# Performance work log

Measured on AMD Instinct MI355X. Metric: run time of the kernel, lower is better.

The kernel has to match this reference:

```python
import jax, jax.numpy as jnp
import numpy as np


def setup_inputs() -> dict:
    key = jax.random.key(0)
    ks = jax.random.split(key, 7)
    N, D, C, SY, SX = 512, 256, 128, 12, 12
    return {
        "f_t": jax.random.normal(ks[0], (N, D), dtype=jnp.float32),
        "fmap_t": jax.random.normal(ks[1], (N, SY, SX, C), dtype=jnp.float32),
        "fmap_tp1": jax.random.normal(ks[2], (N, SY, SX, C), dtype=jnp.float32),
        "W1": jax.random.normal(ks[3], (C, D), dtype=jnp.float32) * 0.05,
        "b1": jax.random.normal(ks[4], (C,), dtype=jnp.float32) * 0.05,
        "W2": jax.random.normal(ks[5], (C, C), dtype=jnp.float32) * 0.05,
        "b2": jax.random.normal(ks[6], (C,), dtype=jnp.float32) * 0.05,
    }


def _ce_diag(logits):
    # logits: [L, N, N]; labels are arange(N) per location.
    lse = jax.nn.logsumexp(logits, axis=-1)           # [L, N]
    diag = jnp.diagonal(logits, axis1=1, axis2=2)     # [L, N]
    # mean over batch per location, then mean over locations == sum/L in torch code
    return jnp.mean(lse - diag)


def reference(f_t, fmap_t, fmap_tp1, W1, b1, W2, b2):
    N = f_t.shape[0]
    C = fmap_tp1.shape[-1]
    # flatten spatial grid: [L, N, C]
    pos = fmap_tp1.reshape(N, -1, C).transpose(1, 0, 2)
    loc = fmap_t.reshape(N, -1, C).transpose(1, 0, 2)

    # loss1: global-local. classifier1(f_t) is loop-invariant -> computed once.
    preds1 = f_t @ W1.T + b1                          # [N, C]
    logits1 = jnp.einsum('nc,lmc->lnm', preds1, pos)  # [L, N, N]
    loss1 = _ce_diag(logits1)

    # loss2: local-local, per-location linear fused as batched einsum.
    preds2 = jnp.einsum('lnc,dc->lnd', loc, W2) + b2  # [L, N, C]
    logits2 = jnp.einsum('lnc,lmc->lnm', preds2, pos) # [L, N, N]
    loss2 = _ce_diag(logits2)

    return loss1 + loss2
```

## Files before the change

### kernel.cpp

```cpp
#include <hip/hip_runtime.h>
#include <hip/hip_bf16.h>
#include <math.h>

#define LC 18432
#define LOG2E 1.4426950408889634f

typedef short bf16x8 __attribute__((ext_vector_type(8)));
typedef float f32x4 __attribute__((ext_vector_type(4)));

#define MFMA16 __builtin_amdgcn_mfma_f32_16x16x32_bf16

__device__ __forceinline__ float fast_exp2(float x) {
#if __has_builtin(__builtin_amdgcn_exp2f)
  return __builtin_amdgcn_exp2f(x);
#else
  return exp2f(x);
#endif
}
__device__ __forceinline__ float fast_log2(float x) {
#if __has_builtin(__builtin_amdgcn_logf)
  return __builtin_amdgcn_logf(x);
#else
  return log2f(x);
#endif
}

__device__ __forceinline__ ushort f2bf(float x) {
  __hip_bfloat16 h = __float2bfloat16(x);
  return __builtin_bit_cast(ushort, h);
}

__device__ __forceinline__ int swb(int row, int x) {
  return (row << 8) + (x ^ ((row & 15) << 4));
}
__device__ __forceinline__ int swb9(int row, int x) {
  return (row << 9) + (x ^ ((row & 15) << 4));
}

__global__ __launch_bounds__(256) void preds1_k(
    const float* __restrict__ f_t, const float* __restrict__ W1,
    const float* __restrict__ b1, ushort* __restrict__ p1img,
    float* __restrict__ out) {
  if (blockIdx.x == 0 && threadIdx.x == 0) *out = 0.f;
  __shared__ __align__(16) ushort sF[32 * 256];
  __shared__ __align__(16) ushort sW[64 * 256];
  const int rc = blockIdx.x >> 1, dh = blockIdx.x & 1;
  const int t = threadIdx.x;
  const int wave = t >> 6, lane = t & 63, lo = lane & 15, hi = lane >> 4;
#pragma unroll
  for (int k = 0; k < 8; ++k) {
    int idx = t + k * 256;
    int row = idx >> 6, c4 = (idx & 63) << 2;
    float4 v = *(const float4*)(f_t + (size_t)(rc * 32 + row) * 256 + c4);
    ushort4 h = {f2bf(v.x), f2bf(v.y), f2bf(v.z), f2bf(v.w)};
    *(ushort4*)((char*)sF + swb9(row, c4 << 1)) = h;
  }
#pragma unroll
  for (int k = 0; k < 16; ++k) {
    int idx = t + k * 256;
    int row = idx >> 6, c4 = (idx & 63) << 2;
    float4 v = *(const float4*)(W1 + (size_t)(dh * 64 + row) * 256 + c4);
    ushort4 h = {f2bf(v.x), f2bf(v.y), f2bf(v.z), f2bf(v.w)};
    *(ushort4*)((char*)sW + swb9(row, c4 << 1)) = h;
  }
  __syncthreads();
  const int rn = (wave & 1) * 16, wd = (wave >> 1) * 32;
  f32x4 acc[2] = {};
#pragma unroll
  for (int s = 0; s < 8; ++s) {
    int x = s * 64 + hi * 16;
    bf16x8 a = *(const bf16x8*)((const char*)sF + swb9(rn + lo, x));
#pragma unroll
    for (int j = 0; j < 2; ++j) {
      bf16x8 b = *(const bf16x8*)((const char*)sW + swb9(wd + j * 16 + lo, x));
      acc[j] = MFMA16(a, b, acc[j], 0, 0, 0);
    }
  }
#pragma unroll
  for (int j = 0; j < 2; ++j) {
    int d = dh * 64 + wd + j * 16 + lo;
    float bb = b1[d];
#pragma unroll
    for (int e = 0; e < 4; ++e) {
      int R = rc * 32 + rn + hi * 4 + e;
      int tile = R >> 6, rin = R & 63;
      *(ushort*)((char*)p1img + (size_t)tile * 16384 + (rin << 8) +
                 ((2 * d) ^ ((rin & 15) << 4))) =
          f2bf((acc[j][e] + bb) * LOG2E);
    }
  }
}

__device__ __forceinline__ void load_tile(float4 pv[4], const float* __restrict__ base,
                                          int t) {
#pragma unroll
  for (int k = 0; k < 4; ++k) {
    int idx = t + k * 512;
    int row = idx >> 5, c4 = (idx & 31) << 2;
    pv[k] = *(const float4*)(base + (size_t)row * LC + c4);
  }
}
__device__ __forceinline__ void write_tile(ushort* dstbuf, const float4 pv[4], int t) {
#pragma unroll
  for (int k = 0; k < 4; ++k) {
    int idx = t + k * 512;
    int row = idx >> 5, c4 = (idx & 31) << 2;
    ushort4 h = {f2bf(pv[k].x), f2bf(pv[k].y), f2bf(pv[k].z), f2bf(pv[k].w)};
    *(ushort4*)((char*)dstbuf + swb(row, c4 << 1)) = h;
  }
}

__global__ __launch_bounds__(512) void stdim_fused(
    const ushort* __restrict__ p1img, const float* __restrict__ fmap_t,
    const float* __restrict__ fmap_tp1, const float* __restrict__ W2,
    const float* __restrict__ b2, float* __restrict__ out) {
  __shared__ __align__(16) ushort sP[8192];
  __shared__ __align__(16) ushort sPos[16384];
  __shared__ float s_rows[2][64][2];
  __shared__ float s_diag[2][64];
  __shared__ float s_red[8];

  const int bid = blockIdx.x;
  const int work = (bid & 7) * 144 + (bid >> 3);
  const int l = work >> 3, rb = work & 7;
  const int t = threadIdx.x;
  const int wave = t >> 6, lane = t & 63, lo = lane & 15, hi = lane >> 4;
  const int ty_ = wave >> 2, wr = (wave >> 1) & 1, wc = wave & 1;

  const float* posbase = fmap_tp1 + l * 128;

#pragma unroll
  for (int k = 0; k < 4; ++k) {
    int idx = t + k * 512;
    int row = idx >> 5, c4 = (idx & 31) << 2;
    float4 v = *(const float4*)(fmap_t + (size_t)(rb * 64 + row) * LC + l * 128 + c4);
    ushort4 h = {f2bf(v.x), f2bf(v.y), f2bf(v.z), f2bf(v.w)};
    *(ushort4*)((char*)sP + swb(row, c4 << 1)) = h;
  }
#pragma unroll
  for (int k = 0; k < 8; ++k) {
    int idx = t + k * 512;
    int row = idx >> 5, c4 = (idx & 31) << 2;
    float4 v = *(const float4*)(W2 + (size_t)row * 128 + c4);
    ushort4 h = {f2bf(v.x), f2bf(v.y), f2bf(v.z), f2bf(v.w)};
    *(ushort4*)((char*)sPos + swb(row, c4 << 1)) = h;
  }
  const int wn = (wave & 1) * 32, wd = (wave >> 1) * 32;
  const float b2a = b2[wd + lo], b2b = b2[wd + 16 + lo];
  float4 pvA[4], pvB[4];
  load_tile(pvA, posbase, t);
  load_tile(pvB, posbase + (size_t)64 * LC, t);
  __syncthreads();

  f32x4 acc2[2][2] = {};
#pragma unroll
  for (int s = 0; s < 4; ++s) {
    int x = s * 64 + hi * 16;
    bf16x8 a0 = *(const bf16x8*)((const char*)sP + swb(wn + lo, x));
    bf16x8 a1 = *(const bf16x8*)((const char*)sP + swb(wn + 16 + lo, x));
#pragma unroll
    for (int j = 0; j < 2; ++j) {
      bf16x8 b = *(const bf16x8*)((const char*)sPos + swb(wd + j * 16 + lo, x));
      acc2[0][j] = MFMA16(a0, b, acc2[0][j], 0, 0, 0);
      acc2[1][j] = MFMA16(a1, b, acc2[1][j], 0, 0, 0);
    }
  }
  __syncthreads();

#pragma unroll
  for (int i2 = 0; i2 < 2; ++i2)
#pragma unroll
    for (int j = 0; j < 2; ++j)
#pragma unroll
      for (int e = 0; e < 4; ++e) {
        int r = wn + i2 * 16 + hi * 4 + e;
        int d = wd + j * 16 + lo;
        *(ushort*)((char*)sP + (r << 8) + ((2 * d) ^ ((r & 15) << 4))) =
            f2bf((acc2[i2][j][e] + (j ? b2b : b2a)) * LOG2E);
      }
  write_tile((ushort*)sPos, pvA, t);
  write_tile((ushort*)((char*)sPos + 16384), pvB, t);
  __syncthreads();

  bf16x8 af[2][4];
  if (ty_ == 0) {
    const char* aimg = (const char*)(p1img + (size_t)rb * 8192);
#pragma unroll
    for (int rt = 0; rt < 2; ++rt)
#pragma unroll
      for (int s = 0; s < 4; ++s)
        af[rt][s] = *(const bf16x8*)(aimg + swb(wr * 32 + rt * 16 + lo, s * 64 + hi * 16));
  } else {
#pragma unroll
    for (int rt = 0; rt < 2; ++rt)
#pragma unroll
      for (int s = 0; s < 4; ++s)
        af[rt][s] = *(const bf16x8*)((const char*)sP +
                                     swb(wr * 32 + rt * 16 + lo, s * 64 + hi * 16));
  }

  float sm0[4] = {0.f, 0.f, 0.f, 0.f}, sm1[4] = {0.f, 0.f, 0.f, 0.f};

#pragma unroll
  for (int mt = 0; mt < 8; ++mt) {
    float4 nv[4];
    if (mt < 6) load_tile(nv, posbase + (size_t)((mt + 2) * 64) * LC, t);

    const char* cur = (const char*)sPos + (mt & 1) * 16384;
    f32x4 a00 = {}, a01 = {}, a10 = {}, a11 = {};
#pragma unroll
    for (int s = 0; s < 4; ++s) {
      int x = s * 64 + hi * 16;
      bf16x8 b0 = *(const bf16x8*)(cur + swb(wc * 32 + lo, x));
      bf16x8 b1 = *(const bf16x8*)(cur + swb(wc * 32 + 16 + lo, x));
      a00 = MFMA16(af[0][s], b0, a00, 0, 0, 0);
      a01 = MFMA16(af[0][s], b1, a01, 0, 0, 0);
      a10 = MFMA16(af[1][s], b0, a10, 0, 0, 0);
      a11 = MFMA16(af[1][s], b1, a11, 0, 0, 0);
    }
#pragma unroll
    for (int i = 0; i < 4; ++i) {
      sm0[i] += fast_exp2(a00[i]) + fast_exp2(a01[i]);
      sm1[i] += fast_exp2(a10[i]) + fast_exp2(a11[i]);
    }
    if (mt == rb && wc == wr) {
#pragma unroll
      for (int i = 0; i < 4; ++i) {
        if (lo == hi * 4 + i) {
          s_diag[ty_][wr * 32 + hi * 4 + i] = a00[i];
          s_diag[ty_][wr * 32 + 16 + hi * 4 + i] = a11[i];
        }
      }
    }
    __syncthreads();
    if (mt < 6)
      write_tile((ushort*)((char*)sPos + (mt & 1) * 16384), nv, t);
  }

#pragma unroll
  for (int i = 0; i < 4; ++i) {
    float v0 = sm0[i], v1 = sm1[i];
#pragma unroll
    for (int st = 1; st <= 8; st <<= 1) {
      v0 += __shfl_xor(v0, st);
      v1 += __shfl_xor(v1, st);
    }
    sm0[i] = v0;
    sm1[i] = v1;
  }
  if (lo == 0) {
#pragma unroll
    for (int i = 0; i < 4; ++i) {
      s_rows[ty_][wr * 32 + hi * 4 + i][wc] = sm0[i];
      s_rows[ty_][wr * 32 + 16 + hi * 4 + i][wc] = sm1[i];
    }
  }
  __syncthreads();

  float part = 0.f;
  if (t < 128) {
    int ty = t >> 6, r = t & 63;
    float tot = s_rows[ty][r][0] + s_rows[ty][r][1];
    part = fast_log2(tot) - s_diag[ty][r];
  }
#pragma unroll
  for (int st = 1; st <= 32; st <<= 1) part += __shfl_xor(part, st);
  if (lane == 0) s_red[wave] = part;
  __syncthreads();
  if (t == 0) {
    float s = 0.f;
#pragma unroll
    for (int w = 0; w < 8; ++w) s += s_red[w];
    atomicAdd(out, s * (0.6931471805599453f / 73728.0f));
  }
}

extern "C" void kernel_launch(void* const* d_in, const int* in_sizes, int n_in,
                              void* d_out, int out_size, void* d_ws, size_t ws_size,
                              hipStream_t stream) {
  const float* f_t      = (const float*)d_in[0];
  const float* fmap_t   = (const float*)d_in[1];
  const float* fmap_tp1 = (const float*)d_in[2];
  const float* W1       = (const float*)d_in[3];
  const float* b1       = (const float*)d_in[4];
  const float* W2       = (const float*)d_in[5];
  const float* b2       = (const float*)d_in[6];
  float* out = (float*)d_out;
  ushort* p1img = (ushort*)d_ws;

  preds1_k<<<32, 256, 0, stream>>>(f_t, W1, b1, p1img, out);
  stdim_fused<<<1152, 512, 0, stream>>>(p1img, fmap_t, fmap_tp1, W2, b2, out);
}
```

Before: 153.7 us.

## Pre-convert positive feature maps to swizzled bf16 and stream them via global_load_lds

Adds a prep kernel that converts each fmap_tp1 tile to a swizzled bf16 image in workspace once. The main kernel then streams these tiles straight into LDS with async global_load_lds double buffering instead of loading fp32 into registers and converting, which is repeated by every row-block (8x). LDS use shrinks by splitting the W2 load into two halves across wave groups, allowing a 6-blocks occupancy hint, and MFMA sections get raised priority. The cost is an extra workspace round-trip and more barriers in the W2 stage.

```diff
diff --git a/kernel.cpp b/kernel.cpp
--- a/kernel.cpp
+++ b/kernel.cpp
@@ -9,6 +9,7 @@
 typedef float f32x4 __attribute__((ext_vector_type(4)));
 
 #define MFMA16 __builtin_amdgcn_mfma_f32_16x16x32_bf16
+#define WAITVM0 asm volatile("s_waitcnt vmcnt(0)" ::: "memory")
 
 __device__ __forceinline__ float fast_exp2(float x) {
 #if __has_builtin(__builtin_amdgcn_exp2f)
@@ -37,85 +38,87 @@
   return (row << 9) + (x ^ ((row & 15) << 4));
 }
 
-__global__ __launch_bounds__(256) void preds1_k(
-    const float* __restrict__ f_t, const float* __restrict__ W1,
-    const float* __restrict__ b1, ushort* __restrict__ p1img,
+typedef const __attribute__((address_space(1))) unsigned int g_u32;
+typedef __attribute__((address_space(3))) unsigned int l_u32;
+__device__ __forceinline__ void gl_lds16(const ushort* g, ushort* l) {
+  __builtin_amdgcn_global_load_lds((g_u32*)g, (l_u32*)l, 16, 0, 0);
+}
+
+__global__ __launch_bounds__(256) void prep_all(
+    const float* __restrict__ f_t, const float* __restrict__ fmap_tp1,
+    const float* __restrict__ W1, const float* __restrict__ b1,
+    ushort* __restrict__ p1img, ushort* __restrict__ posimg,
     float* __restrict__ out) {
-  if (blockIdx.x == 0 && threadIdx.x == 0) *out = 0.f;
-  __shared__ __align__(16) ushort sF[32 * 256];
-  __shared__ __align__(16) ushort sW[64 * 256];
-  const int rc = blockIdx.x >> 1, dh = blockIdx.x & 1;
-  const int t = threadIdx.x;
+  const int bid = blockIdx.x, t = threadIdx.x;
+  if (bid == 0 && t == 0) *out = 0.f;
   const int wave = t >> 6, lane = t & 63, lo = lane & 15, hi = lane >> 4;
-#pragma unroll
-  for (int k = 0; k < 8; ++k) {
-    int idx = t + k * 256;
-    int row = idx >> 6, c4 = (idx & 63) << 2;
-    float4 v = *(const float4*)(f_t + (size_t)(rc * 32 + row) * 256 + c4);
-    ushort4 h = {f2bf(v.x), f2bf(v.y), f2bf(v.z), f2bf(v.w)};
-    *(ushort4*)((char*)sF + swb9(row, c4 << 1)) = h;
-  }
-#pragma unroll
-  for (int k = 0; k < 16; ++k) {
-    int idx = t + k * 256;
-    int row = idx >> 6, c4 = (idx & 63) << 2;
-    float4 v = *(const float4*)(W1 + (size_t)(dh * 64 + row) * 256 + c4);
-    ushort4 h = {f2bf(v.x), f2bf(v.y), f2bf(v.z), f2bf(v.w)};
-    *(ushort4*)((char*)sW + swb9(row, c4 << 1)) = h;
-  }
-  __syncthreads();
-  const int rn = (wave & 1) * 16, wd = (wave >> 1) * 32;
-  f32x4 acc[2] = {};
-#pragma unroll
-  for (int s = 0; s < 8; ++s) {
-    int x = s * 64 + hi * 16;
-    bf16x8 a = *(const bf16x8*)((const char*)sF + swb9(rn + lo, x));
+
+  if (bid < 32) {
+    __shared__ __align__(16) ushort sF[32 * 256];
+    __shared__ __align__(16) ushort sW[64 * 256];
+    const int rc = bid >> 1, dh = bid & 1;
+#pragma unroll
+    for (int k = 0; k < 8; ++k) {
+      int idx = t + k * 256;
+      int row = idx >> 6, c4 = (idx & 63) << 2;
+      float4 v = *(const float4*)(f_t + (size_t)(rc * 32 + row) * 256 + c4);
+      ushort4 h = {f2bf(v.x), f2bf(v.y), f2bf(v.z), f2bf(v.w)};
+      *(ushort4*)((char*)sF + swb9(row, c4 << 1)) = h;
+    }
+#pragma unroll
+    for (int k = 0; k < 16; ++k) {
+      int idx = t + k * 256;
+      int row = idx >> 6, c4 = (idx & 63) << 2;
+      float4 v = *(const float4*)(W1 + (size_t)(dh * 64 + row) * 256 + c4);
+      ushort4 h = {f2bf(v.x), f2bf(v.y), f2bf(v.z), f2bf(v.w)};
+      *(ushort4*)((char*)sW + swb9(row, c4 << 1)) = h;
+    }
+    __syncthreads();
+    const int rn = (wave & 1) * 16, wd = (wave >> 1) * 32;
+    f32x4 acc[2] = {};
+#pragma unroll
+    for (int s = 0; s < 8; ++s) {
+      int x = s * 64 + hi * 16;
+      bf16x8 a = *(const bf16x8*)((const char*)sF + swb9(rn + lo, x));
+#pragma unroll
+      for (int j = 0; j < 2; ++j) {
+        bf16x8 b = *(const bf16x8*)((const char*)sW + swb9(wd + j * 16 + lo, x));
+        acc[j] = MFMA16(a, b, acc[j], 0, 0, 0);
+      }
+    }
 #pragma unroll
     for (int j = 0; j < 2; ++j) {
-      bf16x8 b = *(const bf16x8*)((const char*)sW + swb9(wd + j * 16 + lo, x));
-      acc[j] = MFMA16(a, b, acc[j], 0, 0, 0);
-    }
-  }
-#pragma unroll
-  for (int j = 0; j < 2; ++j) {
-    int d = dh * 64 + wd + j * 16 + lo;
-    float bb = b1[d];
-#pragma unroll
-    for (int e = 0; e < 4; ++e) {
-      int R = rc * 32 + rn + hi * 4 + e;
-      int tile = R >> 6, rin = R & 63;
-      *(ushort*)((char*)p1img + (size_t)tile * 16384 + (rin << 8) +
-                 ((2 * d) ^ ((rin & 15) << 4))) =
-          f2bf((acc[j][e] + bb) * LOG2E);
-    }
-  }
-}
-
-__device__ __forceinline__ void load_tile(float4 pv[4], const float* __restrict__ base,
-                                          int t) {
-#pragma unroll
-  for (int k = 0; k < 4; ++k) {
-    int idx = t + k * 512;
-    int row = idx >> 5, c4 = (idx & 31) << 2;
-    pv[k] = *(const float4*)(base + (size_t)row * LC + c4);
-  }
-}
-__device__ __forceinline__ void write_tile(ushort* dstbuf, const float4 pv[4], int t) {
-#pragma unroll
-  for (int k = 0; k < 4; ++k) {
-    int idx = t + k * 512;
-    int row = idx >> 5, c4 = (idx & 31) << 2;
-    ushort4 h = {f2bf(pv[k].x), f2bf(pv[k].y), f2bf(pv[k].z), f2bf(pv[k].w)};
-    *(ushort4*)((char*)dstbuf + swb(row, c4 << 1)) = h;
-  }
-}
-
-__global__ __launch_bounds__(512) void stdim_fused(
+      int d = dh * 64 + wd + j * 16 + lo;
+      float bb = b1[d];
+#pragma unroll
+      for (int e = 0; e < 4; ++e) {
+        int R = rc * 32 + rn + hi * 4 + e;
+        int tile = R >> 6, rin = R & 63;
+        *(ushort*)((char*)p1img + (size_t)tile * 16384 + (rin << 8) +
+                   ((2 * d) ^ ((rin & 15) << 4))) =
+            f2bf((acc[j][e] + bb) * LOG2E);
+      }
+    }
+  } else {
+    const int bb = bid - 32;
+    const int l = bb >> 3, mtt = bb & 7;
+    ushort* tile = posimg + (size_t)bb * 8192;
+#pragma unroll
+    for (int k = 0; k < 8; ++k) {
+      int idx = t + k * 256;
+      int row = idx >> 5, c4 = (idx & 31) << 2;
+      float4 v = *(const float4*)(fmap_tp1 + (size_t)(mtt * 64 + row) * LC + l * 128 + c4);
+      ushort4 h = {f2bf(v.x), f2bf(v.y), f2bf(v.z), f2bf(v.w)};
+      *(ushort4*)((char*)tile + swb(row, c4 << 1)) = h;
+    }
+  }
+}
+
+__global__ __launch_bounds__(512, 6) void stdim_fused(
     const ushort* __restrict__ p1img, const float* __restrict__ fmap_t,
-    const float* __restrict__ fmap_tp1, const float* __restrict__ W2,
+    const ushort* __restrict__ posimg, const float* __restrict__ W2,
     const float* __restrict__ b2, float* __restrict__ out) {
-  __shared__ __align__(16) ushort sP[8192];
-  __shared__ __align__(16) ushort sPos[16384];
+  __shared__ __align__(16) ushort sB[2][8192];
   __shared__ float s_rows[2][64][2];
   __shared__ float s_diag[2][64];
   __shared__ float s_red[8];
@@ -127,42 +130,64 @@
   const int wave = t >> 6, lane = t & 63, lo = lane & 15, hi = lane >> 4;
   const int ty_ = wave >> 2, wr = (wave >> 1) & 1, wc = wave & 1;
 
-  const float* posbase = fmap_tp1 + l * 128;
-
 #pragma unroll
   for (int k = 0; k < 4; ++k) {
     int idx = t + k * 512;
     int row = idx >> 5, c4 = (idx & 31) << 2;
     float4 v = *(const float4*)(fmap_t + (size_t)(rb * 64 + row) * LC + l * 128 + c4);
     ushort4 h = {f2bf(v.x), f2bf(v.y), f2bf(v.z), f2bf(v.w)};
-    *(ushort4*)((char*)sP + swb(row, c4 << 1)) = h;
-  }
-#pragma unroll
-  for (int k = 0; k < 8; ++k) {
+    *(ushort4*)((char*)sB[0] + swb(row, c4 << 1)) = h;
+  }
+#pragma unroll
+  for (int k = 0; k < 4; ++k) {
     int idx = t + k * 512;
     int row = idx >> 5, c4 = (idx & 31) << 2;
     float4 v = *(const float4*)(W2 + (size_t)row * 128 + c4);
     ushort4 h = {f2bf(v.x), f2bf(v.y), f2bf(v.z), f2bf(v.w)};
-    *(ushort4*)((char*)sPos + swb(row, c4 << 1)) = h;
+    *(ushort4*)((char*)sB[1] + swb(row, c4 << 1)) = h;
   }
   const int wn = (wave & 1) * 32, wd = (wave >> 1) * 32;
   const float b2a = b2[wd + lo], b2b = b2[wd + 16 + lo];
-  float4 pvA[4], pvB[4];
-  load_tile(pvA, posbase, t);
-  load_tile(pvB, posbase + (size_t)64 * LC, t);
   __syncthreads();
 
   f32x4 acc2[2][2] = {};
-#pragma unroll
-  for (int s = 0; s < 4; ++s) {
-    int x = s * 64 + hi * 16;
-    bf16x8 a0 = *(const bf16x8*)((const char*)sP + swb(wn + lo, x));
-    bf16x8 a1 = *(const bf16x8*)((const char*)sP + swb(wn + 16 + lo, x));
-#pragma unroll
-    for (int j = 0; j < 2; ++j) {
-      bf16x8 b = *(const bf16x8*)((const char*)sPos + swb(wd + j * 16 + lo, x));
-      acc2[0][j] = MFMA16(a0, b, acc2[0][j], 0, 0, 0);
-      acc2[1][j] = MFMA16(a1, b, acc2[1][j], 0, 0, 0);
+  const int wdl = wd & 63;
+  if (wave < 4) {
+#pragma unroll
+    for (int s = 0; s < 4; ++s) {
+      int x = s * 64 + hi * 16;
+      bf16x8 a0 = *(const bf16x8*)((const char*)sB[0] + swb(wn + lo, x));
+      bf16x8 a1 = *(const bf16x8*)((const char*)sB[0] + swb(wn + 16 + lo, x));
+#pragma unroll
+      for (int j = 0; j < 2; ++j) {
+        bf16x8 b = *(const bf16x8*)((const char*)sB[1] + swb(wdl + j * 16 + lo, x));
+        acc2[0][j] = MFMA16(a0, b, acc2[0][j], 0, 0, 0);
+        acc2[1][j] = MFMA16(a1, b, acc2[1][j], 0, 0, 0);
+      }
+    }
+  }
+  __syncthreads();
+#pragma unroll
+  for (int k = 0; k < 4; ++k) {
+    int idx = t + k * 512;
+    int row = idx >> 5, c4 = (idx & 31) << 2;
+    float4 v = *(const float4*)(W2 + (size_t)(64 + row) * 128 + c4);
+    ushort4 h = {f2bf(v.x), f2bf(v.y), f2bf(v.z), f2bf(v.w)};
+    *(ushort4*)((char*)sB[1] + swb(row, c4 << 1)) = h;
+  }
+  __syncthreads();
+  if (wave >= 4) {
+#pragma unroll
+    for (int s = 0; s < 4; ++s) {
+      int x = s * 64 + hi * 16;
+      bf16x8 a0 = *(const bf16x8*)((const char*)sB[0] + swb(wn + lo, x));
+      bf16x8 a1 = *(const bf16x8*)((const char*)sB[0] + swb(wn + 16 + lo, x));
+#pragma unroll
+      for (int j = 0; j < 2; ++j) {
+        bf16x8 b = *(const bf16x8*)((const char*)sB[1] + swb(wdl + j * 16 + lo, x));
+        acc2[0][j] = MFMA16(a0, b, acc2[0][j], 0, 0, 0);
+        acc2[1][j] = MFMA16(a1, b, acc2[1][j], 0, 0, 0);
+      }
     }
   }
   __syncthreads();
@@ -175,11 +200,9 @@
       for (int e = 0; e < 4; ++e) {
         int r = wn + i2 * 16 + hi * 4 + e;
         int d = wd + j * 16 + lo;
-        *(ushort*)((char*)sP + (r << 8) + ((2 * d) ^ ((r & 15) << 4))) =
+        *(ushort*)((char*)sB[0] + (r << 8) + ((2 * d) ^ ((r & 15) << 4))) =
             f2bf((acc2[i2][j][e] + (j ? b2b : b2a)) * LOG2E);
       }
-  write_tile((ushort*)sPos, pvA, t);
-  write_tile((ushort*)((char*)sPos + 16384), pvB, t);
   __syncthreads();
 
   bf16x8 af[2][4];
@@ -195,29 +218,45 @@
     for (int rt = 0; rt < 2; ++rt)
 #pragma unroll
       for (int s = 0; s < 4; ++s)
-        af[rt][s] = *(const bf16x8*)((const char*)sP +
+        af[rt][s] = *(const bf16x8*)((const char*)sB[0] +
                                      swb(wr * 32 + rt * 16 + lo, s * 64 + hi * 16));
   }
+  __syncthreads();
+
+  const ushort* ptile = posimg + (size_t)(l * 8) * 8192;
+  const ushort* gsrc = ptile + wave * 1024 + lane * 8;
+  {
+    ushort* dst = (ushort*)sB[0] + wave * 1024;
+    gl_lds16(gsrc, dst);
+    gl_lds16(gsrc + 512, dst + 512);
+  }
+  WAITVM0;
+  __syncthreads();
 
   float sm0[4] = {0.f, 0.f, 0.f, 0.f}, sm1[4] = {0.f, 0.f, 0.f, 0.f};
 
 #pragma unroll
   for (int mt = 0; mt < 8; ++mt) {
-    float4 nv[4];
-    if (mt < 6) load_tile(nv, posbase + (size_t)((mt + 2) * 64) * LC, t);
-
-    const char* cur = (const char*)sPos + (mt & 1) * 16384;
+    const int cur = mt & 1;
+    if (mt < 7) {
+      const ushort* src = gsrc + (size_t)(mt + 1) * 8192;
+      ushort* dst = (ushort*)sB[cur ^ 1] + wave * 1024;
+      gl_lds16(src, dst);
+      gl_lds16(src + 512, dst + 512);
+    }
     f32x4 a00 = {}, a01 = {}, a10 = {}, a11 = {};
+    __builtin_amdgcn_s_setprio(1);
 #pragma unroll
     for (int s = 0; s < 4; ++s) {
       int x = s * 64 + hi * 16;
-      bf16x8 b0 = *(const bf16x8*)(cur + swb(wc * 32 + lo, x));
-      bf16x8 b1 = *(const bf16x8*)(cur + swb(wc * 32 + 16 + lo, x));
+      bf16x8 b0 = *(const bf16x8*)((const char*)sB[cur] + swb(wc * 32 + lo, x));
+      bf16x8 b1 = *(const bf16x8*)((const char*)sB[cur] + swb(wc * 32 + 16 + lo, x));
       a00 = MFMA16(af[0][s], b0, a00, 0, 0, 0);
       a01 = MFMA16(af[0][s], b1, a01, 0, 0, 0);
       a10 = MFMA16(af[1][s], b0, a10, 0, 0, 0);
       a11 = MFMA16(af[1][s], b1, a11, 0, 0, 0);
     }
+    __builtin_amdgcn_s_setprio(0);
 #pragma unroll
     for (int i = 0; i < 4; ++i) {
       sm0[i] += fast_exp2(a00[i]) + fast_exp2(a01[i]);
@@ -233,8 +272,6 @@
       }
     }
     __syncthreads();
-    if (mt < 6)
-      write_tile((ushort*)((char*)sPos + (mt & 1) * 16384), nv, t);
   }
 
 #pragma unroll
@@ -286,8 +323,10 @@
   const float* W2       = (const float*)d_in[5];
   const float* b2       = (const float*)d_in[6];
   float* out = (float*)d_out;
-  ushort* p1img = (ushort*)d_ws;
-
-  preds1_k<<<32, 256, 0, stream>>>(f_t, W1, b1, p1img, out);
-  stdim_fused<<<1152, 512, 0, stream>>>(p1img, fmap_t, fmap_tp1, W2, b2, out);
-}
+
+  ushort* p1img  = (ushort*)d_ws;
+  ushort* posimg = p1img + 8 * 8192;
+
+  prep_all<<<32 + 1152, 256, 0, stream>>>(f_t, fmap_tp1, W1, b1, p1img, posimg, out);
+  stdim_fused<<<1152, 512, 0, stream>>>(p1img, fmap_t, posimg, W2, b2, out);
+}
```

New measurement: 222.6 us. 44.8% more time.
